# Optimization experiments

Hardware: AMD Instinct MI355X
Metric: run time of the kernel (lower is better)

Reference implementation:

```python
import jax, jax.numpy as jnp
import numpy as np
import math

N_EMBD = 1024
N_HEAD = 16
HEAD = N_EMBD // N_HEAD
LAMBDA_INIT = 0.8 - 0.6 * math.exp(-0.3 * (4 - 1))  # layer_idx=4
EPS = 1e-5


def setup_inputs() -> dict:
    key = jax.random.key(0)
    ks = jax.random.split(key, 12)
    s = 1.0 / math.sqrt(N_EMBD)
    inp = {
        "x": jax.random.normal(ks[0], (2, 2048, N_EMBD), dtype=jnp.float32),
        "q1_w": jax.random.normal(ks[1], (N_EMBD, N_EMBD), dtype=jnp.float32) * s,
        "q2_w": jax.random.normal(ks[2], (N_EMBD, N_EMBD), dtype=jnp.float32) * s,
        "k1_w": jax.random.normal(ks[3], (N_EMBD, N_EMBD), dtype=jnp.float32) * s,
        "k2_w": jax.random.normal(ks[4], (N_EMBD, N_EMBD), dtype=jnp.float32) * s,
        "v_w": jax.random.normal(ks[5], (N_EMBD, 2 * N_EMBD), dtype=jnp.float32) * s,
        "c_w": jax.random.normal(ks[6], (2 * N_EMBD, N_EMBD), dtype=jnp.float32) * (1.0 / math.sqrt(2 * N_EMBD)),
        "lambda_q1": jax.random.normal(ks[7], (N_HEAD, HEAD), dtype=jnp.float32) * 0.1,
        "lambda_k1": jax.random.normal(ks[8], (N_HEAD, HEAD), dtype=jnp.float32) * 0.1,
        "lambda_q2": jax.random.normal(ks[9], (N_HEAD, HEAD), dtype=jnp.float32) * 0.1,
        "lambda_k2": jax.random.normal(ks[10], (N_HEAD, HEAD), dtype=jnp.float32) * 0.1,
    }
    return inp


def reference(x, q1_w, q2_w, k1_w, k2_w, v_w, c_w,
              lambda_q1, lambda_k1, lambda_q2, lambda_k2):
    B, T, C = x.shape
    H, hs = N_HEAD, HEAD

    def heads(w, d):
        return (x @ w).reshape(B, T, H, d).transpose(0, 2, 1, 3)  # [B,H,T,d]

    q1 = heads(q1_w, hs)
    q2 = heads(q2_w, hs)
    k1 = heads(k1_w, hs)
    k2 = heads(k2_w, hs)
    v = heads(v_w, 2 * hs)  # [B,H,T,2*hs]

    scale = 1.0 / math.sqrt(hs)
    causal = jnp.tril(jnp.ones((T, T), dtype=bool))  # [T,T]
    neg = jnp.float32(-jnp.inf)

    att1 = jnp.einsum('bhqd,bhkd->bhqk', q1, k1) * scale
    att2 = jnp.einsum('bhqd,bhkd->bhqk', q2, k2) * scale
    att1 = jax.nn.softmax(jnp.where(causal, att1, neg), axis=-1)
    att2 = jax.nn.softmax(jnp.where(causal, att2, neg), axis=-1)

    lam1 = jnp.exp(jnp.sum(lambda_q1 * lambda_k1, axis=-1))  # [H]
    lam2 = jnp.exp(jnp.sum(lambda_q2 * lambda_k2, axis=-1))  # [H]
    lam = (lam1 - lam2 + LAMBDA_INIT)[None, :, None, None]

    att = att1 - lam * att2
    y = jnp.einsum('bhqk,bhkd->bhqd', att, v)  # [B,H,T,2*hs]

    # per-head LayerNorm over 2*hs, no affine
    mu = jnp.mean(y, axis=-1, keepdims=True)
    var = jnp.mean(jnp.square(y - mu), axis=-1, keepdims=True)
    y = (y - mu) / jnp.sqrt(var + EPS)
    y = y * (1.0 - LAMBDA_INIT)

    y = y.transpose(0, 2, 1, 3).reshape(B, T, 2 * C)
    return y @ c_w
```

## Files before the change

### kernel.cpp

```cpp
#include <hip/hip_runtime.h>
#include <cstdint>
#include <cstddef>

typedef __bf16 bf16;
typedef __bf16 bf16x8 __attribute__((ext_vector_type(8)));
typedef __bf16 bf16x4 __attribute__((ext_vector_type(4)));
typedef float f32x4 __attribute__((ext_vector_type(4)));

#define LAMBDA_INIT_F 0.5560582041556405f
#define ONE_MINUS_LI_F 0.4439417958443595f

static constexpr int T = 2048;
static constexpr int ROWQ = 6144;

__device__ __forceinline__ f32x4 mfma16(bf16x8 a, bf16x8 b, f32x4 c) {
  return __builtin_amdgcn_mfma_f32_16x16x32_bf16(a, b, c, 0, 0, 0);
}

__device__ __forceinline__ void gld16(const bf16* g, bf16* l) {
  __builtin_amdgcn_global_load_lds(
      (const __attribute__((address_space(1))) void*)g,
      (__attribute__((address_space(3))) void*)l, 16, 0, 0);
}


__global__ void cvt_f32_bf16(const float* __restrict__ src, bf16* __restrict__ dst, int n4) {
  int i = blockIdx.x * blockDim.x + threadIdx.x;
  if (i < n4) {
    float4 v = reinterpret_cast<const float4*>(src)[i];
    bf16x4 o;
    o[0] = (bf16)v.x; o[1] = (bf16)v.y; o[2] = (bf16)v.z; o[3] = (bf16)v.w;
    reinterpret_cast<bf16x4*>(dst)[i] = o;
  }
}

__global__ void transpose_cvt(const float* __restrict__ src, bf16* __restrict__ dst,
                              int K, int N) {
  __shared__ float t[32][33];
  int tx = threadIdx.x, ty = threadIdx.y;
  int n0 = blockIdx.x * 32, k0 = blockIdx.y * 32;
#pragma unroll
  for (int j = 0; j < 32; j += 8)
    t[ty + j][tx] = src[(size_t)(k0 + ty + j) * N + n0 + tx];
  __syncthreads();
#pragma unroll
  for (int j = 0; j < 32; j += 8)
    dst[(size_t)(n0 + ty + j) * K + k0 + tx] = (bf16)t[tx][ty + j];
}

__global__ void vtrans(const bf16* __restrict__ qkv, bf16* __restrict__ Vt) {
  __shared__ bf16 tile[64][72];
  const int tid = threadIdx.x;
  const int t0 = blockIdx.x * 64, dt = blockIdx.y, bh = blockIdx.z;
  const int b = bh >> 4, h = bh & 15;
#pragma unroll
  for (int i = 0; i < 2; ++i) {
    int S = tid + i * 256;
    int r = S >> 3, c = S & 7;
    *reinterpret_cast<bf16x8*>(&tile[r][c * 8]) =
        *reinterpret_cast<const bf16x8*>(
            &qkv[(size_t)(b * T + t0 + r) * ROWQ + 4096 + h * 128 + dt * 64 + c * 8]);
  }
  __syncthreads();
#pragma unroll
  for (int i = 0; i < 2; ++i) {
    int S = tid + i * 256;
    int dr = S >> 3, tc = S & 7;
    bf16x8 v;
#pragma unroll
    for (int j = 0; j < 8; ++j) v[j] = tile[tc * 8 + j][dr];
    *reinterpret_cast<bf16x8*>(
        &Vt[((size_t)bh * 128 + dt * 64 + dr) * 2048 + t0 + tc * 8]) = v;
  }
}


template <typename OutT>
__global__ __launch_bounds__(256, 2) void gemm_bt(const bf16* __restrict__ A,
                                                  const bf16* __restrict__ Bt,
                                                  OutT* __restrict__ C,
                                                  int M, int N, int K) {
  __shared__ __align__(16) bf16 As[2][128 * 64];
  __shared__ __align__(16) bf16 Bs[2][128 * 64];
  const int tid = threadIdx.x;
  const int lane = tid & 63;
  const int wv = tid >> 6;
  const int wr = wv >> 1, wc = wv & 1;
  const int bm = blockIdx.y * 128, bn = blockIdx.x * 128;
  const int lr = lane & 15, lg = lane >> 4;

  f32x4 acc[4][4] = {};
  const int KT = K >> 6;

#define STAGE_AB(buf, kk0)                                                      \
  do {                                                                          \
    _Pragma("unroll") for (int i_ = 0; i_ < 4; ++i_) {                          \
      int S_ = (i_ * 4 + wv) * 64 + lane;                                       \
      int rw_ = S_ >> 3;                                                        \
      int cg_ = (S_ & 7) ^ (rw_ & 7);                                           \
      gld16(&A[(size_t)(bm + rw_) * K + (kk0) + cg_ * 8], &As[buf][(i_ * 4 + wv) * 512]); \
      gld16(&Bt[(size_t)(bn + rw_) * K + (kk0) + cg_ * 8], &Bs[buf][(i_ * 4 + wv) * 512]); \
    }                                                                           \
  } while (0)

  STAGE_AB(0, 0);
  for (int kt = 0; kt < KT; ++kt) {
    const int cur = kt & 1;
    asm volatile("s_waitcnt vmcnt(0)" ::: "memory");
    __syncthreads();
    if (kt + 1 < KT) STAGE_AB(cur ^ 1, (kt + 1) * 64);
#pragma unroll
    for (int kh = 0; kh < 2; ++kh) {
      bf16x8 af[4], bfr[4];
#pragma unroll
      for (int m = 0; m < 4; ++m)
        af[m] = *reinterpret_cast<const bf16x8*>(
            &As[cur][(wr * 64 + m * 16 + lr) * 64 + (((kh * 4 + lg) ^ (lr & 7)) * 8)]);
#pragma unroll
      for (int n = 0; n < 4; ++n)
        bfr[n] = *reinterpret_cast<const bf16x8*>(
            &Bs[cur][(wc * 64 + n * 16 + lr) * 64 + (((kh * 4 + lg) ^ (lr & 7)) * 8)]);
#pragma unroll
      for (int m = 0; m < 4; ++m)
#pragma unroll
        for (int n = 0; n < 4; ++n)
          acc[m][n] = mfma16(af[m], bfr[n], acc[m][n]);
    }
  }
#undef STAGE_AB

#pragma unroll
  for (int m = 0; m < 4; ++m)
#pragma unroll
    for (int n = 0; n < 4; ++n)
#pragma unroll
      for (int r = 0; r < 4; ++r) {
        int row = bm + wr * 64 + m * 16 + lg * 4 + r;
        int col = bn + wc * 64 + n * 16 + lr;
        C[(size_t)row * N + col] = (OutT)acc[m][n][r];
      }
}


__global__ __launch_bounds__(256, 2) void diff_attn(const bf16* __restrict__ qkv,
                                                    const bf16* __restrict__ Vtg,
                                                    const float* __restrict__ lq1,
                                                    const float* __restrict__ lk1,
                                                    const float* __restrict__ lq2,
                                                    const float* __restrict__ lk2,
                                                    bf16* __restrict__ yln) {
  constexpr int LDP = 72;
  __shared__ __align__(16) bf16 K1s[2][64 * 64];
  __shared__ __align__(16) bf16 K2s[2][64 * 64];
  __shared__ __align__(16) bf16 Vs[2][128 * 64];
  __shared__ __align__(16) bf16 Ps[4][16 * LDP];

  const int fi = blockIdx.x;
  const int bh = blockIdx.y;
  const int b = bh >> 4, h = bh & 15;
  const int tid = threadIdx.x, lane = tid & 63, wv = tid >> 6;
  const int lr = lane & 15, lg = lane >> 4;
  const int qtA = 31 - fi;
  const int qtB = fi;

  const int q1c = h * 64;
  const int q2c = 1024 + h * 64;
  const int k1c = 2048 + h * 64;
  const int k2c = 3072 + h * 64;

  float a1 = lq1[h * 64 + lane] * lk1[h * 64 + lane];
  float a2 = lq2[h * 64 + lane] * lk2[h * 64 + lane];
#pragma unroll
  for (int m = 32; m >= 1; m >>= 1) {
    a1 += __shfl_xor(a1, m);
    a2 += __shfl_xor(a2, m);
  }
  const float lam = __expf(a1) - __expf(a2) + LAMBDA_INIT_F;

  bf16x8 onesf;
#pragma unroll
  for (int j = 0; j < 8; ++j) onesf[j] = (bf16)1.0f;

  bf16x8 q1fA[2], q2fA[2], q1fB[2], q2fB[2];
  {
    const bf16* qa = qkv + (size_t)(b * T + qtA * 64 + wv * 16 + lr) * ROWQ;
    const bf16* qb = qkv + (size_t)(b * T + qtB * 64 + wv * 16 + lr) * ROWQ;
#pragma unroll
    for (int kc = 0; kc < 2; ++kc) {
      q1fA[kc] = *reinterpret_cast<const bf16x8*>(qa + q1c + kc * 32 + lg * 8);
      q2fA[kc] = *reinterpret_cast<const bf16x8*>(qa + q2c + kc * 32 + lg * 8);
      q1fB[kc] = *reinterpret_cast<const bf16x8*>(qb + q1c + kc * 32 + lg * 8);
      q2fB[kc] = *reinterpret_cast<const bf16x8*>(qb + q2c + kc * 32 + lg * 8);
    }
  }

  f32x4 o1A[8] = {}, o2A[8] = {}, o1B[8] = {}, o2B[8] = {};
  f32x4 lA1 = {}, lA2 = {}, lB1 = {}, lB2 = {};

#define STAGE_KV(buf, tt0)                                                       \
  do {                                                                           \
    const bf16* kb_ = qkv + (size_t)(b * T + (tt0)) * ROWQ;                      \
    _Pragma("unroll") for (int i_ = 0; i_ < 2; ++i_) {                           \
      int S_ = (i_ * 4 + wv) * 64 + lane;                                        \
      int rw_ = S_ >> 3;                                                         \
      int cg_ = (S_ & 7) ^ (rw_ & 7);                                            \
      gld16(kb_ + (size_t)rw_ * ROWQ + k1c + cg_ * 8, &K1s[buf][(i_ * 4 + wv) * 512]); \
      gld16(kb_ + (size_t)rw_ * ROWQ + k2c + cg_ * 8, &K2s[buf][(i_ * 4 + wv) * 512]); \
    }                                                                            \
    _Pragma("unroll") for (int i_ = 0; i_ < 4; ++i_) {                           \
      int S_ = (i_ * 4 + wv) * 64 + lane;                                        \
      int dd_ = S_ >> 3;                                                         \
      int cg_ = (S_ & 7) ^ (dd_ & 7);                                            \
      gld16(Vtg + ((size_t)bh * 128 + dd_) * 2048 + (tt0) + cg_ * 8,             \
            &Vs[buf][(i_ * 4 + wv) * 512]);                                      \
    }                                                                            \
  } while (0)

#define ATT_STEP(q1f_, q2f_, o1_, o2_, l1_, l2_, edge_)                          \
  do {                                                                           \
    f32x4 s1_[4] = {}, s2_[4] = {};                                              \
    _Pragma("unroll") for (int n_ = 0; n_ < 4; ++n_) {                           \
      int krow_ = n_ * 16 + lr;                                                  \
      _Pragma("unroll") for (int kc_ = 0; kc_ < 2; ++kc_) {                      \
        bf16x8 kf1_ = *reinterpret_cast<const bf16x8*>(                          \
            &K1s[cur][krow_ * 64 + (((kc_ * 4 + lg) ^ (lr & 7)) * 8)]);          \
        bf16x8 kf2_ = *reinterpret_cast<const bf16x8*>(                          \
            &K2s[cur][krow_ * 64 + (((kc_ * 4 + lg) ^ (lr & 7)) * 8)]);          \
        s1_[n_] = mfma16(q1f_[kc_], kf1_, s1_[n_]);                              \
        s2_[n_] = mfma16(q2f_[kc_], kf2_, s2_[n_]);                              \
      }                                                                          \
    }                                                                            \
    _Pragma("unroll") for (int n_ = 0; n_ < 4; ++n_)                             \
    _Pragma("unroll") for (int r_ = 0; r_ < 4; ++r_) {                           \
      float e1_ = fmaf(s1_[n_][r_], 0.125f, -16.0f);                             \
      float e2_ = fmaf(s2_[n_][r_], 0.125f, -16.0f);                             \
      if (edge_) {                                                               \
        int qq_ = wv * 16 + lg * 4 + r_;                                         \
        int kk_ = n_ * 16 + lr;                                                  \
        if (kk_ > qq_) { e1_ = -1e4f; e2_ = -1e4f; }                             \
      }                                                                          \
      s1_[n_][r_] = __expf(e1_);                                                 \
      s2_[n_][r_] = __expf(e2_);                                                 \
    }                                                                            \
    bf16* Pw_ = &Ps[wv][0];                                                      \
    bf16x8 pa1_[2], pa2_[2];                                                     \
    _Pragma("unroll") for (int n_ = 0; n_ < 4; ++n_)                             \
    _Pragma("unroll") for (int r_ = 0; r_ < 4; ++r_)                             \
        Pw_[(lg * 4 + r_) * LDP + n_ * 16 + lr] = (bf16)s1_[n_][r_];             \
    _Pragma("unroll") for (int kc_ = 0; kc_ < 2; ++kc_)                          \
        pa1_[kc_] = *reinterpret_cast<const bf16x8*>(&Pw_[lr * LDP + kc_ * 32 + lg * 8]); \
    _Pragma("unroll") for (int n_ = 0; n_ < 4; ++n_)                             \
    _Pragma("unroll") for (int r_ = 0; r_ < 4; ++r_)                             \
        Pw_[(lg * 4 + r_) * LDP + n_ * 16 + lr] = (bf16)s2_[n_][r_];             \
    _Pragma("unroll") for (int kc_ = 0; kc_ < 2; ++kc_)                          \
        pa2_[kc_] = *reinterpret_cast<const bf16x8*>(&Pw_[lr * LDP + kc_ * 32 + lg * 8]); \
    _Pragma("unroll") for (int kc_ = 0; kc_ < 2; ++kc_) {                        \
      l1_ = mfma16(pa1_[kc_], onesf, l1_);                                       \
      l2_ = mfma16(pa2_[kc_], onesf, l2_);                                       \
      _Pragma("unroll") for (int nf_ = 0; nf_ < 8; ++nf_) {                      \
        int dd_ = nf_ * 16 + lr;                                                 \
        bf16x8 vb_ = *reinterpret_cast<const bf16x8*>(                           \
            &Vs[cur][dd_ * 64 + (((kc_ * 4 + lg) ^ (lr & 7)) * 8)]);             \
        o1_[nf_] = mfma16(pa1_[kc_], vb_, o1_[nf_]);                             \
        o2_[nf_] = mfma16(pa2_[kc_], vb_, o2_[nf_]);                             \
      }                                                                          \
    }                                                                            \
  } while (0)

  STAGE_KV(0, 0);
  for (int kt = 0; kt <= qtA; ++kt) {
    const int cur = kt & 1;
    asm volatile("s_waitcnt vmcnt(0)" ::: "memory");
    __syncthreads();
    if (kt < qtA) STAGE_KV(cur ^ 1, (kt + 1) * 64);
    ATT_STEP(q1fA, q2fA, o1A, o2A, lA1, lA2, (kt == qtA));
    if (kt <= qtB) ATT_STEP(q1fB, q2fB, o1B, o2B, lB1, lB2, (kt == qtB));
  }
#undef ATT_STEP
#undef STAGE_KV

#define ATT_EPI(o1_, o2_, l1_, l2_, qt_)                                         \
  do {                                                                           \
    float sum_[4] = {}, sq_[4] = {};                                             \
    float i1_[4], i2_[4];                                                        \
    _Pragma("unroll") for (int r_ = 0; r_ < 4; ++r_) {                           \
      i1_[r_] = 1.f / l1_[r_];                                                   \
      i2_[r_] = lam / l2_[r_];                                                   \
    }                                                                            \
    _Pragma("unroll") for (int nf_ = 0; nf_ < 8; ++nf_)                          \
    _Pragma("unroll") for (int r_ = 0; r_ < 4; ++r_) {                           \
      float v_ = o1_[nf_][r_] * i1_[r_] - o2_[nf_][r_] * i2_[r_];                \
      o1_[nf_][r_] = v_;                                                         \
      sum_[r_] += v_;                                                            \
      sq_[r_] += v_ * v_;                                                        \
    }                                                                            \
    _Pragma("unroll") for (int r_ = 0; r_ < 4; ++r_)                             \
    _Pragma("unroll") for (int mm_ = 8; mm_ >= 1; mm_ >>= 1) {                   \
      sum_[r_] += __shfl_xor(sum_[r_], mm_);                                     \
      sq_[r_] += __shfl_xor(sq_[r_], mm_);                                       \
    }                                                                            \
    _Pragma("unroll") for (int r_ = 0; r_ < 4; ++r_) {                           \
      float mu_ = sum_[r_] * (1.f / 128.f);                                      \
      float var_ = sq_[r_] * (1.f / 128.f) - mu_ * mu_;                          \
      float rs_ = rsqrtf(var_ + 1e-5f) * ONE_MINUS_LI_F;                         \
      int row_ = b * T + (qt_)*64 + wv * 16 + lg * 4 + r_;                       \
      bf16* orow_ = yln + (size_t)row_ * 2048 + h * 128;                         \
      _Pragma("unroll") for (int nf_ = 0; nf_ < 8; ++nf_)                        \
          orow_[nf_ * 16 + lr] = (bf16)((o1_[nf_][r_] - mu_) * rs_);             \
    }                                                                            \
  } while (0)

  ATT_EPI(o1A, o2A, lA1, lA2, qtA);
  ATT_EPI(o1B, o2B, lB1, lB2, qtB);
#undef ATT_EPI
}


extern "C" void kernel_launch(void* const* d_in, const int* in_sizes, int n_in,
                              void* d_out, int out_size, void* d_ws, size_t ws_size,
                              hipStream_t stream) {
  const float* x   = (const float*)d_in[0];
  const float* q1w = (const float*)d_in[1];
  const float* q2w = (const float*)d_in[2];
  const float* k1w = (const float*)d_in[3];
  const float* k2w = (const float*)d_in[4];
  const float* vw  = (const float*)d_in[5];
  const float* cw  = (const float*)d_in[6];
  const float* lq1 = (const float*)d_in[7];
  const float* lk1 = (const float*)d_in[8];
  const float* lq2 = (const float*)d_in[9];
  const float* lk2 = (const float*)d_in[10];
  float* out = (float*)d_out;

  char* ws = (char*)d_ws;
  bf16* qkv = (bf16*)(ws);
  bf16* Wt  = (bf16*)(ws + 50331648);
  bf16* xb  = (bf16*)(ws + 62914560);
  bf16* cwt = (bf16*)(ws + 71303168);
  bf16* yln = (bf16*)(ws + 75497472);
  bf16* Vt  = (bf16*)(ws + 50331648);

  cvt_f32_bf16<<<4096, 256, 0, stream>>>(x, xb, 4096 * 1024 / 4);

  dim3 tb(32, 8);
  transpose_cvt<<<dim3(32, 32), tb, 0, stream>>>(q1w, Wt,               1024, 1024);
  transpose_cvt<<<dim3(32, 32), tb, 0, stream>>>(q2w, Wt + 1024 * 1024, 1024, 1024);
  transpose_cvt<<<dim3(32, 32), tb, 0, stream>>>(k1w, Wt + 2048 * 1024, 1024, 1024);
  transpose_cvt<<<dim3(32, 32), tb, 0, stream>>>(k2w, Wt + 3072 * 1024, 1024, 1024);
  transpose_cvt<<<dim3(64, 32), tb, 0, stream>>>(vw,  Wt + 4096 * 1024, 1024, 2048);
  transpose_cvt<<<dim3(32, 64), tb, 0, stream>>>(cw,  cwt,              2048, 1024);

  gemm_bt<bf16><<<dim3(48, 32), 256, 0, stream>>>(xb, Wt, qkv, 4096, 6144, 1024);

  vtrans<<<dim3(32, 2, 32), 256, 0, stream>>>(qkv, Vt);

  diff_attn<<<dim3(16, 32), 256, 0, stream>>>(qkv, Vt, lq1, lk1, lq2, lk2, yln);

  gemm_bt<float><<<dim3(8, 32), 256, 0, stream>>>(yln, cwt, out, 4096, 1024, 2048);
}
```

Before: 218.5 us.

## Rewrite differential attention with 32x32 MFMA, register-resident P, per-wave query tiles

The attention kernel moves from 16x16x32 to 32x32x16 MFMA and computes S transposed (K as the A operand), so the softmax probabilities can be repacked into the PV operand in registers via a cross-half shuffle. This removes the shared-memory P round trip and the ones-vector MFMA row sums. Each wave now owns 32 rows of a single query tile instead of interleaving two tiles per wave. The exp is folded into exp2 with prescaled constants, MFMA sections get raised priority, and tile pairing alternates with batch. Risks are load imbalance between waves sharing a block (A-tile waves do more iterations while B waves idle at barriers) and higher register pressure from 16-wide accumulators.

```diff
diff --git a/kernel.cpp b/kernel.cpp
--- a/kernel.cpp
+++ b/kernel.cpp
@@ -6,21 +6,38 @@
 typedef __bf16 bf16x8 __attribute__((ext_vector_type(8)));
 typedef __bf16 bf16x4 __attribute__((ext_vector_type(4)));
 typedef float f32x4 __attribute__((ext_vector_type(4)));
+typedef float f32x16 __attribute__((ext_vector_type(16)));
 
 #define LAMBDA_INIT_F 0.5560582041556405f
 #define ONE_MINUS_LI_F 0.4439417958443595f
 
 static constexpr int T = 2048;
 static constexpr int ROWQ = 6144;
+#define C1_EXP2 0.18033688011116027f
+#define C0_EXP2 -23.083120654223414f
 
 __device__ __forceinline__ f32x4 mfma16(bf16x8 a, bf16x8 b, f32x4 c) {
   return __builtin_amdgcn_mfma_f32_16x16x32_bf16(a, b, c, 0, 0, 0);
+}
+__device__ __forceinline__ f32x16 mfma32(bf16x8 a, bf16x8 b, f32x16 c) {
+  return __builtin_amdgcn_mfma_f32_32x32x16_bf16(a, b, c, 0, 0, 0);
 }
 
 __device__ __forceinline__ void gld16(const bf16* g, bf16* l) {
   __builtin_amdgcn_global_load_lds(
       (const __attribute__((address_space(1))) void*)g,
       (__attribute__((address_space(3))) void*)l, 16, 0, 0);
+}
+
+__device__ __forceinline__ unsigned pk2(float a, float b) {
+  unsigned short ua = __builtin_bit_cast(unsigned short, (bf16)a);
+  unsigned short ub = __builtin_bit_cast(unsigned short, (bf16)b);
+  return (unsigned)ua | ((unsigned)ub << 16);
+}
+__device__ __forceinline__ bf16x8 mk8(unsigned a, unsigned b, unsigned c, unsigned d) {
+  union { unsigned u[4]; bf16x8 v; } t;
+  t.u[0] = a; t.u[1] = b; t.u[2] = c; t.u[3] = d;
+  return t.v;
 }
 
 
@@ -149,19 +166,20 @@
                                                     const float* __restrict__ lq2,
                                                     const float* __restrict__ lk2,
                                                     bf16* __restrict__ yln) {
-  constexpr int LDP = 72;
   __shared__ __align__(16) bf16 K1s[2][64 * 64];
   __shared__ __align__(16) bf16 K2s[2][64 * 64];
   __shared__ __align__(16) bf16 Vs[2][128 * 64];
-  __shared__ __align__(16) bf16 Ps[4][16 * LDP];
-
-  const int fi = blockIdx.x;
+
+  const int x = blockIdx.x;
   const int bh = blockIdx.y;
   const int b = bh >> 4, h = bh & 15;
   const int tid = threadIdx.x, lane = tid & 63, wv = tid >> 6;
-  const int lr = lane & 15, lg = lane >> 4;
-  const int qtA = 31 - fi;
-  const int qtB = fi;
+  const int lc = lane & 31, hi = lane >> 5;
+
+  const int u = b ? x : 15 - x;
+  const int qtA = 31 - u, qtB = u;
+  const int qt_w = (wv < 2) ? qtA : qtB;
+  const int qbase = qt_w * 64 + (wv & 1) * 32;
 
   const int q1c = h * 64;
   const int q2c = 1024 + h * 64;
@@ -177,25 +195,18 @@
   }
   const float lam = __expf(a1) - __expf(a2) + LAMBDA_INIT_F;
 
-  bf16x8 onesf;
-#pragma unroll
-  for (int j = 0; j < 8; ++j) onesf[j] = (bf16)1.0f;
-
-  bf16x8 q1fA[2], q2fA[2], q1fB[2], q2fB[2];
+  bf16x8 q1f[4], q2f[4];
   {
-    const bf16* qa = qkv + (size_t)(b * T + qtA * 64 + wv * 16 + lr) * ROWQ;
-    const bf16* qb = qkv + (size_t)(b * T + qtB * 64 + wv * 16 + lr) * ROWQ;
-#pragma unroll
-    for (int kc = 0; kc < 2; ++kc) {
-      q1fA[kc] = *reinterpret_cast<const bf16x8*>(qa + q1c + kc * 32 + lg * 8);
-      q2fA[kc] = *reinterpret_cast<const bf16x8*>(qa + q2c + kc * 32 + lg * 8);
-      q1fB[kc] = *reinterpret_cast<const bf16x8*>(qb + q1c + kc * 32 + lg * 8);
-      q2fB[kc] = *reinterpret_cast<const bf16x8*>(qb + q2c + kc * 32 + lg * 8);
+    const bf16* qrow = qkv + (size_t)(b * T + qbase + lc) * ROWQ;
+#pragma unroll
+    for (int kc = 0; kc < 4; ++kc) {
+      q1f[kc] = *reinterpret_cast<const bf16x8*>(qrow + q1c + kc * 16 + hi * 8);
+      q2f[kc] = *reinterpret_cast<const bf16x8*>(qrow + q2c + kc * 16 + hi * 8);
     }
   }
 
-  f32x4 o1A[8] = {}, o2A[8] = {}, o1B[8] = {}, o2B[8] = {};
-  f32x4 lA1 = {}, lA2 = {}, lB1 = {}, lB2 = {};
+  f32x16 o1[4] = {}, o2[4] = {};
+  float l1 = 0.f, l2 = 0.f;
 
 #define STAGE_KV(buf, tt0)                                                       \
   do {                                                                           \
@@ -216,54 +227,45 @@
     }                                                                            \
   } while (0)
 
-#define ATT_STEP(q1f_, q2f_, o1_, o2_, l1_, l2_, edge_)                          \
+#define QK_MAT(Ks, qf, pa, lacc)                                                 \
   do {                                                                           \
-    f32x4 s1_[4] = {}, s2_[4] = {};                                              \
-    _Pragma("unroll") for (int n_ = 0; n_ < 4; ++n_) {                           \
-      int krow_ = n_ * 16 + lr;                                                  \
-      _Pragma("unroll") for (int kc_ = 0; kc_ < 2; ++kc_) {                      \
-        bf16x8 kf1_ = *reinterpret_cast<const bf16x8*>(                          \
-            &K1s[cur][krow_ * 64 + (((kc_ * 4 + lg) ^ (lr & 7)) * 8)]);          \
-        bf16x8 kf2_ = *reinterpret_cast<const bf16x8*>(                          \
-            &K2s[cur][krow_ * 64 + (((kc_ * 4 + lg) ^ (lr & 7)) * 8)]);          \
-        s1_[n_] = mfma16(q1f_[kc_], kf1_, s1_[n_]);                              \
-        s2_[n_] = mfma16(q2f_[kc_], kf2_, s2_[n_]);                              \
+    f32x16 s0 = {}, s1 = {};                                                     \
+    _Pragma("unroll") for (int kc = 0; kc < 4; ++kc) {                           \
+      int g_ = (((kc * 2 + hi) ^ (lc & 7)) * 8);                                 \
+      bf16x8 kf0 = *reinterpret_cast<const bf16x8*>(&Ks[cur][lc * 64 + g_]);     \
+      bf16x8 kf1 = *reinterpret_cast<const bf16x8*>(&Ks[cur][(32 + lc) * 64 + g_]); \
+      s0 = mfma32(kf0, qf[kc], s0);                                              \
+      s1 = mfma32(kf1, qf[kc], s1);                                              \
+    }                                                                            \
+    const int qq_ = qbase + lc;                                                  \
+    _Pragma("unroll") for (int r = 0; r < 16; ++r) {                             \
+      int kl_ = kt * 64 + (r & 3) + 8 * (r >> 2) + 4 * hi;                       \
+      float e0 = fmaf(s0[r], C1_EXP2, C0_EXP2);                                  \
+      float e1 = fmaf(s1[r], C1_EXP2, C0_EXP2);                                  \
+      if (edge) {                                                                \
+        if (kl_ > qq_) e0 = -10000.f;                                            \
+        if (kl_ + 32 > qq_) e1 = -10000.f;                                       \
       }                                                                          \
-    }                                                                            \
-    _Pragma("unroll") for (int n_ = 0; n_ < 4; ++n_)                             \
-    _Pragma("unroll") for (int r_ = 0; r_ < 4; ++r_) {                           \
-      float e1_ = fmaf(s1_[n_][r_], 0.125f, -16.0f);                             \
-      float e2_ = fmaf(s2_[n_][r_], 0.125f, -16.0f);                             \
-      if (edge_) {                                                               \
-        int qq_ = wv * 16 + lg * 4 + r_;                                         \
-        int kk_ = n_ * 16 + lr;                                                  \
-        if (kk_ > qq_) { e1_ = -1e4f; e2_ = -1e4f; }                             \
-      }                                                                          \
-      s1_[n_][r_] = __expf(e1_);                                                 \
-      s2_[n_][r_] = __expf(e2_);                                                 \
-    }                                                                            \
-    bf16* Pw_ = &Ps[wv][0];                                                      \
-    bf16x8 pa1_[2], pa2_[2];                                                     \
-    _Pragma("unroll") for (int n_ = 0; n_ < 4; ++n_)                             \
-    _Pragma("unroll") for (int r_ = 0; r_ < 4; ++r_)                             \
-        Pw_[(lg * 4 + r_) * LDP + n_ * 16 + lr] = (bf16)s1_[n_][r_];             \
-    _Pragma("unroll") for (int kc_ = 0; kc_ < 2; ++kc_)                          \
-        pa1_[kc_] = *reinterpret_cast<const bf16x8*>(&Pw_[lr * LDP + kc_ * 32 + lg * 8]); \
-    _Pragma("unroll") for (int n_ = 0; n_ < 4; ++n_)                             \
-    _Pragma("unroll") for (int r_ = 0; r_ < 4; ++r_)                             \
-        Pw_[(lg * 4 + r_) * LDP + n_ * 16 + lr] = (bf16)s2_[n_][r_];             \
-    _Pragma("unroll") for (int kc_ = 0; kc_ < 2; ++kc_)                          \
-        pa2_[kc_] = *reinterpret_cast<const bf16x8*>(&Pw_[lr * LDP + kc_ * 32 + lg * 8]); \
-    _Pragma("unroll") for (int kc_ = 0; kc_ < 2; ++kc_) {                        \
-      l1_ = mfma16(pa1_[kc_], onesf, l1_);                                       \
-      l2_ = mfma16(pa2_[kc_], onesf, l2_);                                       \
-      _Pragma("unroll") for (int nf_ = 0; nf_ < 8; ++nf_) {                      \
-        int dd_ = nf_ * 16 + lr;                                                 \
-        bf16x8 vb_ = *reinterpret_cast<const bf16x8*>(                           \
-            &Vs[cur][dd_ * 64 + (((kc_ * 4 + lg) ^ (lr & 7)) * 8)]);             \
-        o1_[nf_] = mfma16(pa1_[kc_], vb_, o1_[nf_]);                             \
-        o2_[nf_] = mfma16(pa2_[kc_], vb_, o2_[nf_]);                             \
-      }                                                                          \
+      s0[r] = exp2f(e0);                                                         \
+      s1[r] = exp2f(e1);                                                         \
+      lacc += s0[r] + s1[r];                                                     \
+    }                                                                            \
+    _Pragma("unroll") for (int kc = 0; kc < 4; ++kc) {                           \
+      int base = 8 * (kc & 1);                                                   \
+      float v0 = (kc < 2) ? s0[base + 0] : s1[base + 0];                         \
+      float v1 = (kc < 2) ? s0[base + 1] : s1[base + 1];                         \
+      float v2 = (kc < 2) ? s0[base + 2] : s1[base + 2];                         \
+      float v3 = (kc < 2) ? s0[base + 3] : s1[base + 3];                         \
+      float v4 = (kc < 2) ? s0[base + 4] : s1[base + 4];                         \
+      float v5 = (kc < 2) ? s0[base + 5] : s1[base + 5];                         \
+      float v6 = (kc < 2) ? s0[base + 6] : s1[base + 6];                         \
+      float v7 = (kc < 2) ? s0[base + 7] : s1[base + 7];                         \
+      unsigned pla = pk2(v0, v1), plb = pk2(v2, v3);                             \
+      unsigned pha = pk2(v4, v5), phb = pk2(v6, v7);                             \
+      unsigned ka = hi ? pha : pla, kb = hi ? phb : plb;                         \
+      unsigned sa = hi ? pla : pha, sb = hi ? plb : phb;                         \
+      unsigned ra = __shfl_xor(sa, 32), rb = __shfl_xor(sb, 32);                 \
+      pa[kc] = hi ? mk8(ra, rb, ka, kb) : mk8(ka, kb, ra, rb);                   \
     }                                                                            \
   } while (0)
 
@@ -273,46 +275,56 @@
     asm volatile("s_waitcnt vmcnt(0)" ::: "memory");
     __syncthreads();
     if (kt < qtA) STAGE_KV(cur ^ 1, (kt + 1) * 64);
-    ATT_STEP(q1fA, q2fA, o1A, o2A, lA1, lA2, (kt == qtA));
-    if (kt <= qtB) ATT_STEP(q1fB, q2fB, o1B, o2B, lB1, lB2, (kt == qtB));
-  }
-#undef ATT_STEP
+    if (kt <= qt_w) {
+      const bool edge = (kt == qt_w);
+      bf16x8 pa1[4], pa2[4];
+      __builtin_amdgcn_s_setprio(1);
+      QK_MAT(K1s, q1f, pa1, l1);
+      QK_MAT(K2s, q2f, pa2, l2);
+#pragma unroll
+      for (int n = 0; n < 4; ++n) {
+        int vr = n * 32 + lc;
+#pragma unroll
+        for (int kc = 0; kc < 4; ++kc) {
+          int g_ = (((kc * 2 + hi) ^ (lc & 7)) * 8);
+          bf16x8 vf = *reinterpret_cast<const bf16x8*>(&Vs[cur][vr * 64 + g_]);
+          o1[n] = mfma32(pa1[kc], vf, o1[n]);
+          o2[n] = mfma32(pa2[kc], vf, o2[n]);
+        }
+      }
+      __builtin_amdgcn_s_setprio(0);
+    }
+  }
+#undef QK_MAT
 #undef STAGE_KV
 
-#define ATT_EPI(o1_, o2_, l1_, l2_, qt_)                                         \
-  do {                                                                           \
-    float sum_[4] = {}, sq_[4] = {};                                             \
-    float i1_[4], i2_[4];                                                        \
-    _Pragma("unroll") for (int r_ = 0; r_ < 4; ++r_) {                           \
-      i1_[r_] = 1.f / l1_[r_];                                                   \
-      i2_[r_] = lam / l2_[r_];                                                   \
-    }                                                                            \
-    _Pragma("unroll") for (int nf_ = 0; nf_ < 8; ++nf_)                          \
-    _Pragma("unroll") for (int r_ = 0; r_ < 4; ++r_) {                           \
-      float v_ = o1_[nf_][r_] * i1_[r_] - o2_[nf_][r_] * i2_[r_];                \
-      o1_[nf_][r_] = v_;                                                         \
-      sum_[r_] += v_;                                                            \
-      sq_[r_] += v_ * v_;                                                        \
-    }                                                                            \
-    _Pragma("unroll") for (int r_ = 0; r_ < 4; ++r_)                             \
-    _Pragma("unroll") for (int mm_ = 8; mm_ >= 1; mm_ >>= 1) {                   \
-      sum_[r_] += __shfl_xor(sum_[r_], mm_);                                     \
-      sq_[r_] += __shfl_xor(sq_[r_], mm_);                                       \
-    }                                                                            \
-    _Pragma("unroll") for (int r_ = 0; r_ < 4; ++r_) {                           \
-      float mu_ = sum_[r_] * (1.f / 128.f);                                      \
-      float var_ = sq_[r_] * (1.f / 128.f) - mu_ * mu_;                          \
-      float rs_ = rsqrtf(var_ + 1e-5f) * ONE_MINUS_LI_F;                         \
-      int row_ = b * T + (qt_)*64 + wv * 16 + lg * 4 + r_;                       \
-      bf16* orow_ = yln + (size_t)row_ * 2048 + h * 128;                         \
-      _Pragma("unroll") for (int nf_ = 0; nf_ < 8; ++nf_)                        \
-          orow_[nf_ * 16 + lr] = (bf16)((o1_[nf_][r_] - mu_) * rs_);             \
-    }                                                                            \
-  } while (0)
-
-  ATT_EPI(o1A, o2A, lA1, lA2, qtA);
-  ATT_EPI(o1B, o2B, lB1, lB2, qtB);
-#undef ATT_EPI
+  l1 += __shfl_xor(l1, 32);
+  l2 += __shfl_xor(l2, 32);
+#pragma unroll
+  for (int r = 0; r < 16; ++r) {
+    int qr = (r & 3) + 8 * (r >> 2) + 4 * hi;
+    float il1 = 1.0f / __shfl(l1, qr);
+    float il2 = lam / __shfl(l2, qr);
+    float y0 = o1[0][r] * il1 - o2[0][r] * il2;
+    float y1 = o1[1][r] * il1 - o2[1][r] * il2;
+    float y2 = o1[2][r] * il1 - o2[2][r] * il2;
+    float y3 = o1[3][r] * il1 - o2[3][r] * il2;
+    float sum = y0 + y1 + y2 + y3;
+    float sq = y0 * y0 + y1 * y1 + y2 * y2 + y3 * y3;
+#pragma unroll
+    for (int mm = 16; mm >= 1; mm >>= 1) {
+      sum += __shfl_xor(sum, mm);
+      sq += __shfl_xor(sq, mm);
+    }
+    float mu = sum * (1.f / 128.f);
+    float var = sq * (1.f / 128.f) - mu * mu;
+    float rs = rsqrtf(var + 1e-5f) * ONE_MINUS_LI_F;
+    bf16* orow = yln + (size_t)(b * T + qbase + qr) * 2048 + h * 128 + lc;
+    orow[0]  = (bf16)((y0 - mu) * rs);
+    orow[32] = (bf16)((y1 - mu) * rs);
+    orow[64] = (bf16)((y2 - mu) * rs);
+    orow[96] = (bf16)((y3 - mu) * rs);
+  }
 }
 
 
```

Result: slower. 336.0 us (+53.8%).
